# Kernel tuning notes

Hardware: AMD Instinct MI355X
Metric: run time of the kernel (lower is better)

Reference implementation:

```python
import jax, jax.numpy as jnp
import numpy as np

PI = float(np.pi)
QDIM = 64  # quantum_dim == state_dim == 2**num_qubits


def setup_inputs() -> dict:
    key = jax.random.key(0)
    ks = jax.random.split(key, 8)
    E, Q = 512, QDIM
    s = 1.0 / np.sqrt(E)
    return {
        "features": jax.random.normal(ks[0], (32, 4096, E), dtype=jnp.float32),
        "W_real": jax.random.normal(ks[1], (E, Q), dtype=jnp.float32) * s,
        "b_real": jnp.zeros((Q,), dtype=jnp.float32),
        "W_imag": jax.random.normal(ks[2], (E, Q), dtype=jnp.float32) * s,
        "b_imag": jnp.zeros((Q,), dtype=jnp.float32),
        "W_p1": jax.random.normal(ks[3], (E, Q), dtype=jnp.float32) * s,
        "b_p1": jnp.zeros((Q,), dtype=jnp.float32),
        "W_p2": jax.random.normal(ks[4], (Q, Q), dtype=jnp.float32) * (1.0 / np.sqrt(Q)),
        "b_p2": jnp.zeros((Q,), dtype=jnp.float32),
        "op_params": jax.random.normal(ks[5], (Q,), dtype=jnp.float32),
    }


def hermitian_operator(p):
    # operator_real: eye with diag replaced by sigmoid(p); off-diag [i,j] = p_i * p_j (symmetric)
    R = p[:, None] * p[None, :]
    d = jnp.arange(QDIM)
    R = R.at[d, d].set(jax.nn.sigmoid(p))
    # operator_imag: [i,j] = p_i - p_j (antisymmetric, zero diag)
    I = p[:, None] - p[None, :]
    return R, I


def reference(features, W_real, b_real, W_imag, b_imag, W_p1, b_p1, W_p2, b_p2, op_params):
    # --- QuantumStateEncoder ---
    r = jnp.tanh(features @ W_real + b_real)              # [B,S,Q]
    im = jnp.tanh(features @ W_imag + b_imag)             # [B,S,Q]
    phases = jnp.tanh(jnp.tanh(features @ W_p1 + b_p1) @ W_p2 + b_p2) * PI
    cr, ci = jnp.cos(phases), jnp.sin(phases)
    rp = r * cr - im * ci
    ip = r * ci + im * cr
    norm = jnp.sqrt(jnp.sum(rp * rp + ip * ip, axis=-1, keepdims=True) + 1e-12)
    rn = rp / norm
    inn = ip / norm
    # --- QuantumOperator (hermitian) ---
    R, I = hermitian_operator(op_params)
    out_r = rn @ R - inn @ I
    out_i = rn @ I + inn @ R
    return out_r, out_i, phases
```

## Files before the change

kernel.cpp:

```cpp
#include <hip/hip_runtime.h>
#include <math.h>

#define PI_F 3.14159265358979323846f

typedef __attribute__((ext_vector_type(8))) short  short8;
typedef __attribute__((ext_vector_type(4))) float  floatx4;

constexpr int E = 512;
constexpr int Q = 64;
constexpr int NCHUNK = E / 32;
constexpr int WS_B_ENTRIES = NCHUNK * 12 * 64;
constexpr int WS_P2_OFF = WS_B_ENTRIES;
constexpr int CHUNK_BYTES = 12 * 64 * 16;

__device__ __forceinline__ unsigned short bf16_rne(float x) {
    unsigned u = __float_as_uint(x);
    unsigned r = u + 0x7fffu + ((u >> 16) & 1u);
    return (unsigned short)(r >> 16);
}

__device__ __forceinline__ void split_bf16_8(const float* v, short8& hi, short8& lo) {
    #pragma unroll
    for (int j = 0; j < 8; ++j) {
        unsigned u  = __float_as_uint(v[j]);
        unsigned rh = (u + 0x7fffu + ((u >> 16) & 1u)) & 0xffff0000u;
        hi[j] = (short)(rh >> 16);
        float res = v[j] - __uint_as_float(rh);
        lo[j] = (short)bf16_rne(res);
    }
}

__device__ __forceinline__ float tanh_fast(float x) {
    const float xc = fminf(fmaxf(x, -15.f), 15.f);
    const float e  = __expf(2.f * xc);
    return (e - 1.f) / (e + 1.f);
}

__device__ __forceinline__ void async_copy16(const void* g, void* l) {
    __builtin_amdgcn_global_load_lds(
        (const __attribute__((address_space(1))) unsigned int*)g,
        (__attribute__((address_space(3))) unsigned int*)l, 16, 0, 0);
}

__global__ void prep_weights(const float* __restrict__ Wr, const float* __restrict__ Wi,
                             const float* __restrict__ Wp1, const float* __restrict__ Wp2,
                             short* __restrict__ ws)
{
    const int e = blockIdx.x * 256 + threadIdx.x;
    const float* W;
    int kbase, n;
    if (e < WS_B_ENTRIES) {
        const int L = e & 63;
        const int f = e >> 6;
        const int tt = f & 3;
        const int g  = f >> 2;
        const int m  = g % 3, c = g / 3;
        W = (m == 0) ? Wr : (m == 1) ? Wi : Wp1;
        n     = tt * 16 + (L & 15);
        kbase = c * 32 + (L >> 4) * 8;
    } else {
        const int e2 = e - WS_B_ENTRIES;
        const int L  = e2 & 63;
        const int tt = (e2 >> 6) & 3;
        const int c2 = e2 >> 8;
        W = Wp2;
        n     = tt * 16 + (L & 15);
        kbase = c2 * 32 + (L >> 4) * 8;
    }
    short8 frag;
    #pragma unroll
    for (int j = 0; j < 8; ++j)
        frag[j] = (short)bf16_rne(W[(kbase + j) * Q + n]);
    *(short8*)(ws + (size_t)e * 8) = frag;
}

__global__ __launch_bounds__(256, 4)
void qi_mfma(const float* __restrict__ feat, const short* __restrict__ wsb,
             const float* __restrict__ br,  const float* __restrict__ bi,
             const float* __restrict__ bp1, const float* __restrict__ bp2,
             const float* __restrict__ op_p,
             float* __restrict__ out, long long nrows)
{
    __shared__ alignas(16) union {
        short wbuf[2][CHUNK_BYTES / 2];
        float tp[4][16][68];
    } sh;

    const int tid = threadIdx.x;
    const int L   = tid & 63;
    const int wv  = tid >> 6;
    const int l15 = L & 15;
    const int q4  = L >> 4;
    const long long rowBase = (long long)blockIdx.x * 64 + wv * 16;

    const float* aptr = feat + (rowBase + l15) * (long long)E + q4 * 8;

    {
        const char* g = (const char*)wsb + (size_t)tid * 16;
        char*       l = (char*)sh.wbuf[0] + (size_t)tid * 16;
        #pragma unroll
        for (int r = 0; r < 3; ++r) async_copy16(g + r * 4096, l + r * 4096);
    }
    floatx4 a0 = *(const floatx4*)aptr;
    floatx4 a1 = *(const floatx4*)(aptr + 4);

    floatx4 acc[12];
    #pragma unroll
    for (int t = 0; t < 12; ++t) acc[t] = (floatx4){0.f, 0.f, 0.f, 0.f};

    __syncthreads();

    int cur = 0;
    for (int c = 0; c < NCHUNK; ++c) {
        floatx4 n0, n1;
        const bool has_next = (c + 1 < NCHUNK);
        if (has_next) {
            const char* g = (const char*)wsb + (size_t)(c + 1) * CHUNK_BYTES + (size_t)tid * 16;
            char*       l = (char*)sh.wbuf[cur ^ 1] + (size_t)tid * 16;
            #pragma unroll
            for (int r = 0; r < 3; ++r) async_copy16(g + r * 4096, l + r * 4096);
            n0 = *(const floatx4*)(aptr + (c + 1) * 32);
            n1 = *(const floatx4*)(aptr + (c + 1) * 32 + 4);
        }

        float av[8];
        #pragma unroll
        for (int j = 0; j < 4; ++j) { av[j] = a0[j]; av[4 + j] = a1[j]; }
        short8 ah, al;
        split_bf16_8(av, ah, al);

        const short8* wl = (const short8*)sh.wbuf[cur];
        #pragma unroll
        for (int mt = 0; mt < 12; ++mt) {
            const short8 bf = wl[mt * 64 + L];
            acc[mt] = __builtin_amdgcn_mfma_f32_16x16x32_bf16(ah, bf, acc[mt], 0, 0, 0);
            acc[mt] = __builtin_amdgcn_mfma_f32_16x16x32_bf16(al, bf, acc[mt], 0, 0, 0);
        }

        __syncthreads();
        if (has_next) { a0 = n0; a1 = n1; }
        cur ^= 1;
    }

    float brv[4], biv[4], bp1v[4], bp2v[4], pv[4], dcv[4];
    #pragma unroll
    for (int t = 0; t < 4; ++t) {
        const int colv = t * 16 + l15;
        brv[t] = br[colv]; biv[t] = bi[colv]; bp1v[t] = bp1[colv]; bp2v[t] = bp2[colv];
        const float p = op_p[colv];
        pv[t]  = p;
        dcv[t] = 1.f / (1.f + __expf(-p)) - p * p;
    }

    float rv[4][4], iv[4][4];
    #pragma unroll
    for (int t = 0; t < 4; ++t)
        #pragma unroll
        for (int g = 0; g < 4; ++g) {
            rv[t][g] = tanh_fast(acc[t][g]     + brv[t]);
            iv[t][g] = tanh_fast(acc[4 + t][g] + biv[t]);
            sh.tp[wv][q4 * 4 + g][t * 16 + l15] = tanh_fast(acc[8 + t][g] + bp1v[t]);
        }
    __syncthreads();

    const short8* wfrag = (const short8*)wsb;
    floatx4 accp2[4];
    #pragma unroll
    for (int t = 0; t < 4; ++t) accp2[t] = (floatx4){0.f, 0.f, 0.f, 0.f};
    #pragma unroll
    for (int c2 = 0; c2 < 2; ++c2) {
        float tv[8];
        {
            const floatx4 t0 = *(const floatx4*)&sh.tp[wv][l15][c2 * 32 + q4 * 8];
            const floatx4 t1 = *(const floatx4*)&sh.tp[wv][l15][c2 * 32 + q4 * 8 + 4];
            #pragma unroll
            for (int j = 0; j < 4; ++j) { tv[j] = t0[j]; tv[4 + j] = t1[j]; }
        }
        short8 th, tl;
        split_bf16_8(tv, th, tl);
        #pragma unroll
        for (int tt = 0; tt < 4; ++tt) {
            const short8 bf = wfrag[(size_t)(WS_P2_OFF + (c2 * 4 + tt) * 64 + L)];
            accp2[tt] = __builtin_amdgcn_mfma_f32_16x16x32_bf16(th, bf, accp2[tt], 0, 0, 0);
            accp2[tt] = __builtin_amdgcn_mfma_f32_16x16x32_bf16(tl, bf, accp2[tt], 0, 0, 0);
        }
    }

    float* __restrict__ outR = out;
    float* __restrict__ outI = out +       nrows * Q;
    float* __restrict__ outP = out + 2LL * nrows * Q;

    float rp[4][4], ip[4][4];
    #pragma unroll
    for (int t = 0; t < 4; ++t)
        #pragma unroll
        for (int g = 0; g < 4; ++g) {
            const float ph = tanh_fast(accp2[t][g] + bp2v[t]) * PI_F;
            const long long row = rowBase + q4 * 4 + g;
            outP[row * Q + t * 16 + l15] = ph;
            const float si = __sinf(ph), co = __cosf(ph);
            rp[t][g] = rv[t][g] * co - iv[t][g] * si;
            ip[t][g] = rv[t][g] * si + iv[t][g] * co;
        }

    #pragma unroll
    for (int g = 0; g < 4; ++g) {
        float n2 = 0.f;
        #pragma unroll
        for (int t = 0; t < 4; ++t) n2 += rp[t][g] * rp[t][g] + ip[t][g] * ip[t][g];
        #pragma unroll
        for (int off = 1; off <= 8; off <<= 1) n2 += __shfl_xor(n2, off);
        const float inv = 1.f / sqrtf(n2 + 1e-12f);

        float dR = 0.f, dI = 0.f, sR = 0.f, sI = 0.f;
        #pragma unroll
        for (int t = 0; t < 4; ++t) {
            rp[t][g] *= inv; ip[t][g] *= inv;
            dR += rp[t][g] * pv[t];  dI += ip[t][g] * pv[t];
            sR += rp[t][g];          sI += ip[t][g];
        }
        #pragma unroll
        for (int off = 1; off <= 8; off <<= 1) {
            dR += __shfl_xor(dR, off); dI += __shfl_xor(dI, off);
            sR += __shfl_xor(sR, off); sI += __shfl_xor(sI, off);
        }

        const long long row = rowBase + q4 * 4 + g;
        #pragma unroll
        for (int t = 0; t < 4; ++t) {
            const long long o = row * Q + t * 16 + l15;
            outR[o] = dR * pv[t] + rp[t][g] * dcv[t] - dI + sI * pv[t];
            outI[o] = dR - sR * pv[t] + ip[t][g] * dcv[t] + dI * pv[t];
        }
    }
}

extern "C" void kernel_launch(void* const* d_in, const int* in_sizes, int n_in,
                              void* d_out, int out_size, void* d_ws, size_t ws_size,
                              hipStream_t stream) {
    const float* feat = (const float*)d_in[0];
    const float* Wr   = (const float*)d_in[1];
    const float* br   = (const float*)d_in[2];
    const float* Wi   = (const float*)d_in[3];
    const float* bi   = (const float*)d_in[4];
    const float* Wp1  = (const float*)d_in[5];
    const float* bp1  = (const float*)d_in[6];
    const float* Wp2  = (const float*)d_in[7];
    const float* bp2  = (const float*)d_in[8];
    const float* opp  = (const float*)d_in[9];

    short* ws = (short*)d_ws;

    const long long nrows = (long long)in_sizes[0] / E;
    const int blocks = (int)(nrows / 64);

    hipLaunchKernelGGL(prep_weights, dim3((WS_B_ENTRIES + 512) / 256), dim3(256), 0, stream,
                       Wr, Wi, Wp1, Wp2, ws);
    hipLaunchKernelGGL(qi_mfma, dim3(blocks), dim3(256), 0, stream,
                       feat, ws, br, bi, bp1, bp2, opp, (float*)d_out, nrows);
}
```

Before: 424.8 us.

## Prefetch feature chunks two ahead with explicit vmcnt waits and barriers

The feature-row loads become a two-deep register ring, so each A fragment is fetched two chunks before use instead of one. The plain __syncthreads is replaced by explicit s_waitcnt vmcnt(2)/vmcnt(0) plus s_barrier with sched_barrier fences. The goal is to keep global loads in flight across the barrier rather than draining them at every chunk. The chunk loop is fully unrolled and launch bounds go from 4 to 5 blocks per CU, which squeezes registers and may cause spills.

```diff
diff --git a/kernel.cpp b/kernel.cpp
--- a/kernel.cpp
+++ b/kernel.cpp
@@ -41,6 +41,21 @@
         (const __attribute__((address_space(1))) unsigned int*)g,
         (__attribute__((address_space(3))) unsigned int*)l, 16, 0, 0);
 }
+
+#define VMEM_ORDER_FENCE() do { \
+    asm volatile("" ::: "memory"); \
+    __builtin_amdgcn_sched_barrier(0); } while (0)
+
+#define WAIT_VMCNT_2() do { \
+    asm volatile("s_waitcnt vmcnt(2)" ::: "memory"); \
+    __builtin_amdgcn_sched_barrier(0); } while (0)
+#define WAIT_VMCNT_0() do { \
+    asm volatile("s_waitcnt vmcnt(0)" ::: "memory"); \
+    __builtin_amdgcn_sched_barrier(0); } while (0)
+
+#define BLOCK_BARRIER() do { \
+    __builtin_amdgcn_s_barrier(); \
+    __builtin_amdgcn_sched_barrier(0); } while (0)
 
 __global__ void prep_weights(const float* __restrict__ Wr, const float* __restrict__ Wi,
                              const float* __restrict__ Wp1, const float* __restrict__ Wp2,
@@ -74,7 +89,7 @@
     *(short8*)(ws + (size_t)e * 8) = frag;
 }
 
-__global__ __launch_bounds__(256, 4)
+__global__ __launch_bounds__(256, 5)
 void qi_mfma(const float* __restrict__ feat, const short* __restrict__ wsb,
              const float* __restrict__ br,  const float* __restrict__ bi,
              const float* __restrict__ bp1, const float* __restrict__ bp2,
@@ -95,41 +110,55 @@
 
     const float* aptr = feat + (rowBase + l15) * (long long)E + q4 * 8;
 
+    floatx4 afut[2][2];
+
     {
-        const char* g = (const char*)wsb + (size_t)tid * 16;
-        char*       l = (char*)sh.wbuf[0] + (size_t)tid * 16;
-        #pragma unroll
-        for (int r = 0; r < 3; ++r) async_copy16(g + r * 4096, l + r * 4096);
-    }
-    floatx4 a0 = *(const floatx4*)aptr;
-    floatx4 a1 = *(const floatx4*)(aptr + 4);
+        const char* g = (const char*)wsb;
+        char*       l = (char*)sh.wbuf[0];
+        #pragma unroll
+        for (int r = 0; r < 3; ++r)
+            async_copy16(g + (size_t)tid * 16 + r * 4096, l + (size_t)tid * 16 + r * 4096);
+    }
+    VMEM_ORDER_FENCE();
+    afut[0][0] = *(const floatx4*)(aptr);
+    afut[0][1] = *(const floatx4*)(aptr + 4);
+    afut[1][0] = *(const floatx4*)(aptr + 32);
+    afut[1][1] = *(const floatx4*)(aptr + 36);
+    VMEM_ORDER_FENCE();
 
     floatx4 acc[12];
     #pragma unroll
     for (int t = 0; t < 12; ++t) acc[t] = (floatx4){0.f, 0.f, 0.f, 0.f};
 
-    __syncthreads();
-
-    int cur = 0;
+    WAIT_VMCNT_2();
+    BLOCK_BARRIER();
+
+    #pragma unroll
     for (int c = 0; c < NCHUNK; ++c) {
-        floatx4 n0, n1;
-        const bool has_next = (c + 1 < NCHUNK);
-        if (has_next) {
-            const char* g = (const char*)wsb + (size_t)(c + 1) * CHUNK_BYTES + (size_t)tid * 16;
-            char*       l = (char*)sh.wbuf[cur ^ 1] + (size_t)tid * 16;
+        const int par = c & 1;
+
+        if (c + 1 < NCHUNK) {
+            const char* g = (const char*)wsb + (size_t)(c + 1) * CHUNK_BYTES;
+            char*       l = (char*)sh.wbuf[(c + 1) & 1];
             #pragma unroll
-            for (int r = 0; r < 3; ++r) async_copy16(g + r * 4096, l + r * 4096);
-            n0 = *(const floatx4*)(aptr + (c + 1) * 32);
-            n1 = *(const floatx4*)(aptr + (c + 1) * 32 + 4);
-        }
+            for (int r = 0; r < 3; ++r)
+                async_copy16(g + (size_t)tid * 16 + r * 4096, l + (size_t)tid * 16 + r * 4096);
+        }
+        VMEM_ORDER_FENCE();
 
         float av[8];
         #pragma unroll
-        for (int j = 0; j < 4; ++j) { av[j] = a0[j]; av[4 + j] = a1[j]; }
+        for (int j = 0; j < 4; ++j) { av[j] = afut[par][0][j]; av[4 + j] = afut[par][1][j]; }
+        if (c + 2 < NCHUNK) {
+            afut[par][0] = *(const floatx4*)(aptr + (c + 2) * 32);
+            afut[par][1] = *(const floatx4*)(aptr + (c + 2) * 32 + 4);
+        }
+        VMEM_ORDER_FENCE();
+
         short8 ah, al;
         split_bf16_8(av, ah, al);
 
-        const short8* wl = (const short8*)sh.wbuf[cur];
+        const short8* wl = (const short8*)sh.wbuf[par];
         #pragma unroll
         for (int mt = 0; mt < 12; ++mt) {
             const short8 bf = wl[mt * 64 + L];
@@ -137,9 +166,8 @@
             acc[mt] = __builtin_amdgcn_mfma_f32_16x16x32_bf16(al, bf, acc[mt], 0, 0, 0);
         }
 
-        __syncthreads();
-        if (has_next) { a0 = n0; a1 = n1; }
-        cur ^= 1;
+        if (c < NCHUNK - 2) { WAIT_VMCNT_2(); } else { WAIT_VMCNT_0(); }
+        BLOCK_BARRIER();
     }
 
     float brv[4], biv[4], bp1v[4], bp2v[4], pv[4], dcv[4];
```

Result: no change. 426.6 us (+0.4%).
